# Performance work log

Hardware: AMD Instinct MI355X
Metric: run time of the kernel (lower is better)

Reference implementation:

```python
import jax, jax.numpy as jnp
import numpy as np

KERNEL_MUL = 2.0
KERNEL_NUM = 5


def setup_inputs() -> dict:
    key = jax.random.key(0)
    k1, k2 = jax.random.split(key)
    source = jax.random.normal(k1, (4096, 256), dtype=jnp.float32)
    target = jax.random.normal(k2, (4096, 256), dtype=jnp.float32)
    return {"source": source, "target": target}


def _mmd(source, target):
    b = source.shape[0]
    total = jnp.concatenate([source, target], axis=0)  # [2N, D]
    n = total.shape[0]
    # pairwise squared L2 via gram trick (avoids O(N^2 * D) intermediate)
    sq = jnp.sum(total * total, axis=1)  # [2N]
    d2 = sq[:, None] + sq[None, :] - 2.0 * (total @ total.T)
    d2 = jnp.maximum(d2, 0.0)  # [2N, 2N]
    # bandwidth from detached distances (matches L2_distance.data)
    bandwidth = jax.lax.stop_gradient(jnp.sum(d2)) / (n * n - n)
    bandwidth = bandwidth / (KERNEL_MUL ** (KERNEL_NUM // 2))
    kernels = jnp.zeros_like(d2)
    for i in range(KERNEL_NUM):
        kernels = kernels + jnp.exp(-d2 / (bandwidth * KERNEL_MUL ** i))
    XX = kernels[:b, :b]
    YY = kernels[b:, b:]
    XY = kernels[:b, b:]
    YX = kernels[b:, :b]
    return jnp.mean(XX + YY - XY - YX)


def reference(source, target):
    return _mmd(source, target)
```

## Files before the change

kernel.cpp:

```cpp
#include <hip/hip_runtime.h>
#include <hip/hip_bf16.h>


#define N_TOTAL 8192
#define B_HALF 4096
#define D_DIM 256
#define TILE 128
#define NTILE 64
#define NTRI 2080
#define BK 32
#define NCHUNK 8

typedef float f32x16 __attribute__((ext_vector_type(16)));
typedef _Float16 f16x8 __attribute__((ext_vector_type(8)));

__device__ __forceinline__ const float* row_base(const float* src, const float* tgt, int r) {
    return (r < B_HALF) ? src + (size_t)r * D_DIM : tgt + (size_t)(r - B_HALF) * D_DIM;
}

__global__ __launch_bounds__(256) void prep_kernel(const float* __restrict__ src,
                                                   const float* __restrict__ tgt,
                                                   _Float16* __restrict__ a16,
                                                   float* __restrict__ sq) {
    int w = threadIdx.x >> 6, lane = threadIdx.x & 63;
    int row = blockIdx.x * 4 + w;
    const float* rp = row_base(src, tgt, row);
    float4 v = ((const float4*)rp)[lane];
    float f[4] = {v.x, v.y, v.z, v.w};
    _Float16 h[4];
    #pragma unroll
    for (int e = 0; e < 4; ++e) h[e] = (_Float16)f[e];
    ((ushort4*)(a16 + (size_t)row * D_DIM))[lane] = *(ushort4*)h;
    float s = f[0]*f[0] + f[1]*f[1] + f[2]*f[2] + f[3]*f[3];
    #pragma unroll
    for (int off = 32; off; off >>= 1) s += __shfl_down(s, off, 64);
    if (lane == 0) sq[row] = s;
}

__global__ __launch_bounds__(256) void colpart_kernel(const float* __restrict__ src,
                                                      const float* __restrict__ tgt,
                                                      float* __restrict__ colpart) {
    int t  = threadIdx.x;
    int r0 = blockIdx.x * 128;
    float s = 0.f;
    for (int r = r0; r < r0 + 128; ++r)
        s += row_base(src, tgt, r)[t];
    colpart[blockIdx.x * D_DIM + t] = s;
}

__global__ __launch_bounds__(256) void bw_kernel(const float* __restrict__ sq,
                                                 const float* __restrict__ colpart,
                                                 float* __restrict__ negc,
                                                 double* __restrict__ accum) {
    __shared__ double red[256];
    int t = threadIdx.x;
    double s = 0.0;
    for (int i = t; i < N_TOTAL; i += 256) s += (double)sq[i];
    red[t] = s;
    __syncthreads();
    for (int off = 128; off; off >>= 1) {
        if (t < off) red[t] += red[t + off];
        __syncthreads();
    }
    double sumsq = red[0];
    __syncthreads();
    float c = 0.f;
    #pragma unroll
    for (int k = 0; k < 64; ++k) c += colpart[k * D_DIM + t];
    red[t] = (double)c * (double)c;
    __syncthreads();
    for (int off = 128; off; off >>= 1) {
        if (t < off) red[t] += red[t + off];
        __syncthreads();
    }
    if (t == 0) {
        double S1 = 2.0 * (double)N_TOTAL * sumsq - 2.0 * red[0];
        double nn = (double)N_TOTAL * (double)N_TOTAL - (double)N_TOTAL;
        double bw = S1 / nn / 4.0;
        negc[0] = (float)(-1.4426950408889634 / (16.0 * bw));
        accum[0] = 0.0;
    }
}

__device__ __forceinline__ void gload_lds16(const void* g, void* l) {
    __builtin_amdgcn_global_load_lds((const __attribute__((address_space(1))) unsigned int*)g,
                                     (__attribute__((address_space(3))) unsigned int*)l,
                                     16, 0, 0);
}

__global__ __launch_bounds__(256, 4) void mmd_mfma(const _Float16* __restrict__ a16,
                                                   const float* __restrict__ sq,
                                                   const float* __restrict__ negc,
                                                   double* __restrict__ accum) {
    __shared__ _Float16 lds[2][2][TILE * BK];
    __shared__ float wsum[4];

    int b  = blockIdx.x;
    int bs = (b & 7) * (NTRI / 8) + (b >> 3);
    int it = 0, cum = 0;
    while (cum + (NTILE - it) <= bs) { cum += NTILE - it; ++it; }
    int jt = it + (bs - cum);

    int tid = threadIdx.x, lane = tid & 63, wid = tid >> 6;
    int wrow = wid >> 1, wcol = wid & 1;
    int rowA = it * TILE, rowB = jt * TILE;
    int c32 = lane & 31, khalf = lane >> 5;

    const _Float16* srcs[2] = { a16 + (size_t)rowA * D_DIM,
                                a16 + (size_t)rowB * D_DIM };

    f32x16 acc[2][2] = {};

    auto STAGE = [&](int kt, int buf) {
        int kc = kt * BK;
        #pragma unroll
        for (int t = 0; t < 2; ++t) {
            #pragma unroll
            for (int lg = 0; lg < 2; ++lg) {
                int ci0 = lg * 256 + wid * 64;
                int ci  = ci0 + lane;
                int r   = ci >> 2;
                int sl  = ci & 3;
                int slin = sl ^ ((r >> 1) & 3);
                gload_lds16(srcs[t] + (size_t)r * D_DIM + kc + slin * 8,
                            &lds[buf][t][ci0 * 8]);
            }
        }
    };

    STAGE(0, 0);
    STAGE(1, 1);

    #pragma unroll 1
    for (int kt = 0; kt < NCHUNK; ++kt) {
        int buf = kt & 1;

        if (kt < NCHUNK - 1) asm volatile("s_waitcnt vmcnt(4)" ::: "memory");
        else                 asm volatile("s_waitcnt vmcnt(0)" ::: "memory");
        __builtin_amdgcn_s_barrier();

        #pragma unroll
        for (int kap = 0; kap < 2; ++kap) {
            int s = kap * 2 + khalf;
            f16x8 af[2], bf[2];
            #pragma unroll
            for (int mt = 0; mt < 2; ++mt) {
                int r  = wrow * 64 + mt * 32 + c32;
                int sp = s ^ ((r >> 1) & 3);
                af[mt] = *(const f16x8*)&lds[buf][0][r * BK + sp * 8];
            }
            #pragma unroll
            for (int nt = 0; nt < 2; ++nt) {
                int r  = wcol * 64 + nt * 32 + c32;
                int sp = s ^ ((r >> 1) & 3);
                bf[nt] = *(const f16x8*)&lds[buf][1][r * BK + sp * 8];
            }
            __builtin_amdgcn_s_setprio(1);
            #pragma unroll
            for (int mt = 0; mt < 2; ++mt)
                #pragma unroll
                for (int nt = 0; nt < 2; ++nt)
                    acc[mt][nt] = __builtin_amdgcn_mfma_f32_32x32x16_f16(af[mt], bf[nt], acc[mt][nt], 0, 0, 0);
            __builtin_amdgcn_s_setprio(0);
        }

        asm volatile("s_waitcnt lgkmcnt(0)" ::: "memory");
        __builtin_amdgcn_s_barrier();

        if (kt + 2 < NCHUNK) STAGE(kt + 2, buf);
    }

    float nc = *negc;
    float sjn[2];
    #pragma unroll
    for (int nt = 0; nt < 2; ++nt)
        sjn[nt] = sq[rowB + wcol * 64 + nt * 32 + c32];
    float tsum = 0.f;
    #pragma unroll
    for (int mt = 0; mt < 2; ++mt) {
        #pragma unroll
        for (int reg = 0; reg < 16; ++reg) {
            int i = rowA + wrow * 64 + mt * 32 + (reg & 3) + 8 * (reg >> 2) + 4 * khalf;
            float si = sq[i];
            #pragma unroll
            for (int nt = 0; nt < 2; ++nt) {
                float d2 = fmaxf(si + sjn[nt] - 2.0f * acc[mt][nt][reg], 0.f);
                float u  = exp2f(nc * d2);
                float u2 = u * u, u4 = u2 * u2, u8 = u4 * u4;
                tsum += u + u2 + u4 + u8 + u8 * u8;
            }
        }
    }
    float scale = (((it < 32) == (jt < 32)) ? 1.f : -1.f) * ((it == jt) ? 1.f : 2.f);
    tsum *= scale;

    #pragma unroll
    for (int off = 32; off; off >>= 1) tsum += __shfl_down(tsum, off, 64);
    if (lane == 0) wsum[wid] = tsum;
    __syncthreads();
    if (tid == 0) {
        float t = wsum[0] + wsum[1] + wsum[2] + wsum[3];
        atomicAdd(accum, (double)t);
    }
}

__global__ void finalize_kernel(const double* __restrict__ accum, float* __restrict__ out) {
    out[0] = (float)(accum[0] / ((double)B_HALF * (double)B_HALF));
}

extern "C" void kernel_launch(void* const* d_in, const int* in_sizes, int n_in,
                              void* d_out, int out_size, void* d_ws, size_t ws_size,
                              hipStream_t stream) {
    const float* src = (const float*)d_in[0];
    const float* tgt = (const float*)d_in[1];
    float* out = (float*)d_out;

    char* ws = (char*)d_ws;
    float*  sq      = (float*)ws;
    float*  colpart = (float*)(ws + 32768);
    float*  negc    = (float*)(ws + 98304);
    double* accum   = (double*)(ws + 98312);
    _Float16* a16   = (_Float16*)(ws + 131072);

    prep_kernel<<<N_TOTAL / 4, 256, 0, stream>>>(src, tgt, a16, sq);
    colpart_kernel<<<64, 256, 0, stream>>>(src, tgt, colpart);
    bw_kernel<<<1, 256, 0, stream>>>(sq, colpart, negc, accum);
    mmd_mfma<<<NTRI, 256, 0, stream>>>(a16, sq, negc, accum);
    finalize_kernel<<<1, 1, 0, stream>>>(accum, out);
}
```

Before: 74.03 us.

## Load MFMA operands directly from global memory and fuse prep with column sums

Measured after the change: 112.9 us. +52.5%, slower.

```diff
diff --git a/kernel.cpp b/kernel.cpp
--- a/kernel.cpp
+++ b/kernel.cpp
@@ -8,8 +8,6 @@
 #define TILE 128
 #define NTILE 64
 #define NTRI 2080
-#define BK 32
-#define NCHUNK 8
 
 typedef float f32x16 __attribute__((ext_vector_type(16)));
 typedef _Float16 f16x8 __attribute__((ext_vector_type(8)));
@@ -21,31 +19,26 @@
 __global__ __launch_bounds__(256) void prep_kernel(const float* __restrict__ src,
                                                    const float* __restrict__ tgt,
                                                    _Float16* __restrict__ a16,
-                                                   float* __restrict__ sq) {
-    int w = threadIdx.x >> 6, lane = threadIdx.x & 63;
-    int row = blockIdx.x * 4 + w;
-    const float* rp = row_base(src, tgt, row);
-    float4 v = ((const float4*)rp)[lane];
-    float f[4] = {v.x, v.y, v.z, v.w};
-    _Float16 h[4];
-    #pragma unroll
-    for (int e = 0; e < 4; ++e) h[e] = (_Float16)f[e];
-    ((ushort4*)(a16 + (size_t)row * D_DIM))[lane] = *(ushort4*)h;
-    float s = f[0]*f[0] + f[1]*f[1] + f[2]*f[2] + f[3]*f[3];
-    #pragma unroll
-    for (int off = 32; off; off >>= 1) s += __shfl_down(s, off, 64);
-    if (lane == 0) sq[row] = s;
-}
-
-__global__ __launch_bounds__(256) void colpart_kernel(const float* __restrict__ src,
-                                                      const float* __restrict__ tgt,
-                                                      float* __restrict__ colpart) {
-    int t  = threadIdx.x;
+                                                   float* __restrict__ sq,
+                                                   float* __restrict__ colpart) {
+    int tid = threadIdx.x, w = tid >> 6, lane = tid & 63;
     int r0 = blockIdx.x * 128;
-    float s = 0.f;
+    #pragma unroll 4
+    for (int i = 0; i < 32; ++i) {
+        int row = r0 + w * 32 + i;
+        const float* rp = row_base(src, tgt, row);
+        float4 v = ((const float4*)rp)[lane];
+        _Float16 h[4] = {(_Float16)v.x, (_Float16)v.y, (_Float16)v.z, (_Float16)v.w};
+        ((ushort4*)(a16 + (size_t)row * D_DIM))[lane] = *(ushort4*)h;
+        float s = v.x*v.x + v.y*v.y + v.z*v.z + v.w*v.w;
+        #pragma unroll
+        for (int off = 32; off; off >>= 1) s += __shfl_down(s, off, 64);
+        if (lane == 0) sq[row] = s;
+    }
+    float c = 0.f;
     for (int r = r0; r < r0 + 128; ++r)
-        s += row_base(src, tgt, r)[t];
-    colpart[blockIdx.x * D_DIM + t] = s;
+        c += row_base(src, tgt, r)[tid];
+    colpart[blockIdx.x * D_DIM + tid] = c;
 }
 
 __global__ __launch_bounds__(256) void bw_kernel(const float* __restrict__ sq,
@@ -82,17 +75,10 @@
     }
 }
 
-__device__ __forceinline__ void gload_lds16(const void* g, void* l) {
-    __builtin_amdgcn_global_load_lds((const __attribute__((address_space(1))) unsigned int*)g,
-                                     (__attribute__((address_space(3))) unsigned int*)l,
-                                     16, 0, 0);
-}
-
-__global__ __launch_bounds__(256, 4) void mmd_mfma(const _Float16* __restrict__ a16,
+__global__ __launch_bounds__(256, 4) void mmd_main(const _Float16* __restrict__ a16,
                                                    const float* __restrict__ sq,
                                                    const float* __restrict__ negc,
                                                    double* __restrict__ accum) {
-    __shared__ _Float16 lds[2][2][TILE * BK];
     __shared__ float wsum[4];
 
     int b  = blockIdx.x;
@@ -106,68 +92,23 @@
     int rowA = it * TILE, rowB = jt * TILE;
     int c32 = lane & 31, khalf = lane >> 5;
 
-    const _Float16* srcs[2] = { a16 + (size_t)rowA * D_DIM,
-                                a16 + (size_t)rowB * D_DIM };
+    const _Float16* A0 = a16 + (size_t)(rowA + wrow * 64 + c32) * D_DIM + khalf * 8;
+    const _Float16* B0 = a16 + (size_t)(rowB + wcol * 64 + c32) * D_DIM + khalf * 8;
 
     f32x16 acc[2][2] = {};
 
-    auto STAGE = [&](int kt, int buf) {
-        int kc = kt * BK;
+    #pragma unroll 4
+    for (int kap = 0; kap < 16; ++kap) {
+        f16x8 af[2], bf[2];
+        af[0] = *(const f16x8*)(A0 + kap * 16);
+        af[1] = *(const f16x8*)(A0 + 32 * D_DIM + kap * 16);
+        bf[0] = *(const f16x8*)(B0 + kap * 16);
+        bf[1] = *(const f16x8*)(B0 + 32 * D_DIM + kap * 16);
         #pragma unroll
-        for (int t = 0; t < 2; ++t) {
+        for (int mt = 0; mt < 2; ++mt)
             #pragma unroll
-            for (int lg = 0; lg < 2; ++lg) {
-                int ci0 = lg * 256 + wid * 64;
-                int ci  = ci0 + lane;
-                int r   = ci >> 2;
-                int sl  = ci & 3;
-                int slin = sl ^ ((r >> 1) & 3);
-                gload_lds16(srcs[t] + (size_t)r * D_DIM + kc + slin * 8,
-                            &lds[buf][t][ci0 * 8]);
-            }
-        }
-    };
-
-    STAGE(0, 0);
-    STAGE(1, 1);
-
-    #pragma unroll 1
-    for (int kt = 0; kt < NCHUNK; ++kt) {
-        int buf = kt & 1;
-
-        if (kt < NCHUNK - 1) asm volatile("s_waitcnt vmcnt(4)" ::: "memory");
-        else                 asm volatile("s_waitcnt vmcnt(0)" ::: "memory");
-        __builtin_amdgcn_s_barrier();
-
-        #pragma unroll
-        for (int kap = 0; kap < 2; ++kap) {
-            int s = kap * 2 + khalf;
-            f16x8 af[2], bf[2];
-            #pragma unroll
-            for (int mt = 0; mt < 2; ++mt) {
-                int r  = wrow * 64 + mt * 32 + c32;
-                int sp = s ^ ((r >> 1) & 3);
-                af[mt] = *(const f16x8*)&lds[buf][0][r * BK + sp * 8];
-            }
-            #pragma unroll
-            for (int nt = 0; nt < 2; ++nt) {
-                int r  = wcol * 64 + nt * 32 + c32;
-                int sp = s ^ ((r >> 1) & 3);
-                bf[nt] = *(const f16x8*)&lds[buf][1][r * BK + sp * 8];
-            }
-            __builtin_amdgcn_s_setprio(1);
-            #pragma unroll
-            for (int mt = 0; mt < 2; ++mt)
-                #pragma unroll
-                for (int nt = 0; nt < 2; ++nt)
-                    acc[mt][nt] = __builtin_amdgcn_mfma_f32_32x32x16_f16(af[mt], bf[nt], acc[mt][nt], 0, 0, 0);
-            __builtin_amdgcn_s_setprio(0);
-        }
-
-        asm volatile("s_waitcnt lgkmcnt(0)" ::: "memory");
-        __builtin_amdgcn_s_barrier();
-
-        if (kt + 2 < NCHUNK) STAGE(kt + 2, buf);
+            for (int nt = 0; nt < 2; ++nt)
+                acc[mt][nt] = __builtin_amdgcn_mfma_f32_32x32x16_f16(af[mt], bf[nt], acc[mt][nt], 0, 0, 0);
     }
 
     float nc = *negc;
@@ -222,9 +163,8 @@
     double* accum   = (double*)(ws + 98312);
     _Float16* a16   = (_Float16*)(ws + 131072);
 
-    prep_kernel<<<N_TOTAL / 4, 256, 0, stream>>>(src, tgt, a16, sq);
-    colpart_kernel<<<64, 256, 0, stream>>>(src, tgt, colpart);
+    prep_kernel<<<64, 256, 0, stream>>>(src, tgt, a16, sq, colpart);
     bw_kernel<<<1, 256, 0, stream>>>(sq, colpart, negc, accum);
-    mmd_mfma<<<NTRI, 256, 0, stream>>>(a16, sq, negc, accum);
+    mmd_main<<<NTRI, 256, 0, stream>>>(a16, sq, negc, accum);
     finalize_kernel<<<1, 1, 0, stream>>>(accum, out);
 }
```
